# Performance work log

Measured on AMD Instinct MI355X. Metric: run time of the kernel, lower is better.

The kernel has to match this reference:

```python
import jax, jax.numpy as jnp
import numpy as np

B, T, D, H = 4, 4096, 2048, 128

def setup_inputs() -> dict:
    key = jax.random.key(0)
    k1, k2, k3, k4 = jax.random.split(key, 4)
    scale = 0.02
    return {
        "x": jax.random.normal(k1, (B, T, D), dtype=jnp.float32),
        "Wq": jax.random.normal(k2, (D, H), dtype=jnp.float32) * scale,
        "Wk": jax.random.normal(k3, (D, H), dtype=jnp.float32) * scale,
        "Wv": jax.random.normal(k4, (D, H), dtype=jnp.float32) * scale,
    }

def reference(x, Wq, Wk, Wv):
    # x: [B,T,D]; projections to [B,T,H]
    q = jnp.einsum('btd,dh->bth', x, Wq)
    k = jnp.einsum('btd,dh->bth', x, Wk)
    v = jnp.einsum('btd,dh->bth', x, Wv)
    scale = 1.0 / jnp.sqrt(jnp.asarray(q.shape[-1], q.dtype))
    scores = jnp.einsum('bth,bsh->bts', q, k) * scale  # [B,T,T]
    t = x.shape[1]
    causal = jnp.tril(jnp.ones((t, t), dtype=bool))
    scores = jnp.where(causal, scores, -jnp.inf)
    weights = jax.nn.softmax(scores, axis=-1)
    # dropout p=0.0 (eval) -> identity
    out = jnp.einsum('bts,bsh->bth', weights, v)
    return out
```

## Files before the change

kernel.cpp:

```cpp
#include <hip/hip_runtime.h>
#include <hip/hip_bf16.h>

#define Bq 4
#define Tq 4096
#define Dq 2048
#define Hq 128
#define Mq (Bq*Tq)
#define CHUNK 16

typedef __attribute__((ext_vector_type(8))) short bf16x8;
typedef __attribute__((ext_vector_type(4))) float f32x4;

static __device__ __forceinline__ short bfbits(float f) {
    union { __hip_bfloat16 h; short s; } u;
    u.h = __float2bfloat16(f);
    return u.s;
}
static __device__ __forceinline__ float bf2f(short s) {
    union { unsigned u; float f; } v;
    v.u = ((unsigned)(unsigned short)s) << 16;
    return v.f;
}
#define WAIT_LDS() __builtin_amdgcn_s_waitcnt(0xC07F)

__global__ __launch_bounds__(256, 1) void wt_kernel(
    const float* __restrict__ Wqp,
    const float* __restrict__ Wkp,
    const float* __restrict__ Wvp,
    short* __restrict__ wTg)
{
    __shared__ short trsp[128][136];
    const int kc = blockIdx.x;
    const int w  = blockIdx.y;
    const float* __restrict__ W = (w == 0) ? Wqp : (w == 1) ? Wkp : Wvp;
    const float scale = (w == 0) ? 0.08838834764831843f : 1.0f;
    const int t = threadIdx.x;

    #pragma unroll
    for (int i = 0; i < 16; i++) {
        int idx = t + i * 256;
        int r = idx >> 5, c4 = idx & 31;
        float4 f = *(const float4*)&W[(size_t)(kc * 128 + r) * Hq + c4 * 4];
        trsp[c4 * 4 + 0][r] = bfbits(f.x * scale);
        trsp[c4 * 4 + 1][r] = bfbits(f.y * scale);
        trsp[c4 * 4 + 2][r] = bfbits(f.z * scale);
        trsp[c4 * 4 + 3][r] = bfbits(f.w * scale);
    }
    __syncthreads();
    #pragma unroll
    for (int i = 0; i < 8; i++) {
        int idx = t + i * 256;
        int h = idx >> 4, c8 = idx & 15;
        *(bf16x8*)&wTg[((size_t)w * 128 + h) * Dq + kc * 128 + c8 * 8] =
            *(bf16x8*)&trsp[h][c8 * 8];
    }
}

__global__ __launch_bounds__(256, 2) void qkv_fused_kernel(
    const float* __restrict__ x,
    const short* __restrict__ wTg,
    short* __restrict__ qg,
    short* __restrict__ kg,
    short* __restrict__ vTt)
{
    __shared__ short smem[32 * 72 + 384 * 72];
    short (*xs)[72]  = (short(*)[72])smem;
    short (*wts)[72] = (short(*)[72])(smem + 32 * 72);

    const int m0 = blockIdx.x * 32;

    const int t    = threadIdx.x;
    const int lane = t & 63;
    const int qw   = t >> 6;
    const int l15  = lane & 15;
    const int quad = lane >> 4;

    f32x4 o[2][6];
    #pragma unroll
    for (int mf = 0; mf < 2; mf++)
        #pragma unroll
        for (int j = 0; j < 6; j++) o[mf][j] = (f32x4){0.f, 0.f, 0.f, 0.f};

    const int xr = t >> 3, xc = (t & 7) * 8;

    float4  xreg[2];
    bf16x8  wreg[12];

    {
        const float* src = x + (size_t)(m0 + xr) * Dq + xc;
        xreg[0] = *(const float4*)(src + 0);
        xreg[1] = *(const float4*)(src + 4);
        #pragma unroll
        for (int i = 0; i < 12; i++) {
            int idx = t + i * 256;
            wreg[i] = *(const bf16x8*)&wTg[(size_t)(idx >> 3) * Dq + (idx & 7) * 8];
        }
        bf16x8 v0;
        v0[0] = bfbits(xreg[0].x); v0[1] = bfbits(xreg[0].y);
        v0[2] = bfbits(xreg[0].z); v0[3] = bfbits(xreg[0].w);
        v0[4] = bfbits(xreg[1].x); v0[5] = bfbits(xreg[1].y);
        v0[6] = bfbits(xreg[1].z); v0[7] = bfbits(xreg[1].w);
        *(bf16x8*)&xs[xr][xc] = v0;
        #pragma unroll
        for (int i = 0; i < 12; i++) {
            int idx = t + i * 256;
            *(bf16x8*)&wts[idx >> 3][(idx & 7) * 8] = wreg[i];
        }
    }
    __syncthreads();

    for (int k0 = 0; k0 < Dq; k0 += 64) {
        if (k0 + 64 < Dq) {
            const float* src = x + (size_t)(m0 + xr) * Dq + k0 + 64 + xc;
            xreg[0] = *(const float4*)(src + 0);
            xreg[1] = *(const float4*)(src + 4);
            #pragma unroll
            for (int i = 0; i < 12; i++) {
                int idx = t + i * 256;
                wreg[i] = *(const bf16x8*)&wTg[(size_t)(idx >> 3) * Dq + k0 + 64 + (idx & 7) * 8];
            }
        }

        #pragma unroll
        for (int kk = 0; kk < 2; kk++) {
            bf16x8 a[2], b[6];
            #pragma unroll
            for (int mf = 0; mf < 2; mf++)
                a[mf] = *(bf16x8*)&xs[mf * 16 + l15][kk * 32 + quad * 8];
            #pragma unroll
            for (int j = 0; j < 6; j++)
                b[j] = *(bf16x8*)&wts[qw * 96 + j * 16 + l15][kk * 32 + quad * 8];
            #pragma unroll
            for (int mf = 0; mf < 2; mf++)
                #pragma unroll
                for (int j = 0; j < 6; j++)
                    o[mf][j] = __builtin_amdgcn_mfma_f32_16x16x32_bf16(
                        a[mf], b[j], o[mf][j], 0, 0, 0);
        }
        __syncthreads();
        if (k0 + 64 < Dq) {
            bf16x8 v0;
            v0[0] = bfbits(xreg[0].x); v0[1] = bfbits(xreg[0].y);
            v0[2] = bfbits(xreg[0].z); v0[3] = bfbits(xreg[0].w);
            v0[4] = bfbits(xreg[1].x); v0[5] = bfbits(xreg[1].y);
            v0[6] = bfbits(xreg[1].z); v0[7] = bfbits(xreg[1].w);
            *(bf16x8*)&xs[xr][xc] = v0;
            #pragma unroll
            for (int i = 0; i < 12; i++) {
                int idx = t + i * 256;
                *(bf16x8*)&wts[idx >> 3][(idx & 7) * 8] = wreg[i];
            }
            __syncthreads();
        }
    }

    {
        short (*e64)[264] = (short(*)[264])smem;
        #pragma unroll
        for (int mf = 0; mf < 2; mf++)
            #pragma unroll
            for (int j = 0; j < 6; j++) {
                int n0 = qw * 96 + j * 16;
                if (n0 < 256) {
                    #pragma unroll
                    for (int reg = 0; reg < 4; reg++)
                        e64[mf * 16 + quad * 4 + reg][n0 + l15] = bfbits(o[mf][j][reg]);
                }
            }
        __syncthreads();
        #pragma unroll
        for (int i = 0; i < 4; i++) {
            int idx = t + i * 256;
            int r = idx >> 5, u = idx & 31;
            int n = u * 8;
            bf16x8 val = *(bf16x8*)&e64[r][n];
            short* dst = (n < 128) ? &qg[(size_t)(m0 + r) * Hq + n]
                                   : &kg[(size_t)(m0 + r) * Hq + (n - 128)];
            *(bf16x8*)dst = val;
        }
    }
    __syncthreads();
    {
        short (*e128)[40] = (short(*)[40])smem;
        #pragma unroll
        for (int mf = 0; mf < 2; mf++)
            #pragma unroll
            for (int j = 0; j < 6; j++) {
                int n0 = qw * 96 + j * 16;
                if (n0 >= 256) {
                    short4 pk;
                    pk.x = bfbits(o[mf][j][0]); pk.y = bfbits(o[mf][j][1]);
                    pk.z = bfbits(o[mf][j][2]); pk.w = bfbits(o[mf][j][3]);
                    *(short4*)&e128[(n0 - 256) + l15][mf * 16 + quad * 4] = pk;
                }
            }
        __syncthreads();
        const int bb   = m0 / Tq;
        const int jt   = (m0 % Tq) >> 6;
        const int moff = m0 & 63;
        #pragma unroll
        for (int i = 0; i < 2; i++) {
            int idx = t + i * 256;
            int h = idx >> 2, u = idx & 3;
            *(bf16x8*)&vTt[(((size_t)bb * (Tq / 64) + jt) * 128 + h) * 64 + moff + u * 8] =
                *(bf16x8*)&e128[h][u * 8];
        }
    }
}

__global__ __launch_bounds__(256, 3) void attn_part_kernel(
    const short* __restrict__ qg, const short* __restrict__ kg,
    const short* __restrict__ vTt,
    short* __restrict__ Opart,
    float* __restrict__ lv)
{
    __shared__ short ks_s[64][136];
    __shared__ short vt_s[128][72];
    __shared__ short ps_s[64][72];

    const int qt = blockIdx.x;
    const int b  = blockIdx.y;
    const int c  = blockIdx.z;
    const int q0 = qt * 64;

    const int lo = c * CHUNK;
    const int hi = min(qt + 1, lo + CHUNK);
    if (lo >= hi) return;

    const int t    = threadIdx.x;
    const int lane = t & 63;
    const int qw   = t >> 6;
    const int l15  = lane & 15;
    const int quad = lane >> 4;

    bf16x8 qf[4];
    {
        const short* qsrc = qg + (size_t)(b * Tq + q0 + qw * 16 + l15) * Hq + quad * 8;
        #pragma unroll
        for (int kk = 0; kk < 4; kk++)
            qf[kk] = *(const bf16x8*)(qsrc + kk * 32);
    }

    float lsum[4] = {0.f, 0.f, 0.f, 0.f};
    f32x4 o[8];
    #pragma unroll
    for (int nf = 0; nf < 8; nf++) o[nf] = (f32x4){0.f, 0.f, 0.f, 0.f};

    bf16x8 kreg[4], vreg[4];
    {
        const size_t kbase = (size_t)(b * Tq + lo * 64) * Hq;
        const short* vsrc = vTt + (((size_t)b * (Tq / 64) + lo) * 128) * 64;
        #pragma unroll
        for (int i = 0; i < 4; i++) {
            int idx = t + i * 256;
            kreg[i] = *(const bf16x8*)&kg[kbase + (size_t)(idx >> 4) * Hq + (idx & 15) * 8];
            vreg[i] = *(const bf16x8*)&vsrc[idx * 8];
        }
        #pragma unroll
        for (int i = 0; i < 4; i++) {
            int idx = t + i * 256;
            *(bf16x8*)&ks_s[idx >> 4][(idx & 15) * 8] = kreg[i];
            *(bf16x8*)&vt_s[idx >> 3][(idx & 7) * 8]  = vreg[i];
        }
    }
    __syncthreads();

    for (int jt = lo; jt < hi; jt++) {
        if (jt + 1 < hi) {
            const size_t kbase = (size_t)(b * Tq + (jt + 1) * 64) * Hq;
            const short* vsrc = vTt + (((size_t)b * (Tq / 64) + jt + 1) * 128) * 64;
            #pragma unroll
            for (int i = 0; i < 4; i++) {
                int idx = t + i * 256;
                kreg[i] = *(const bf16x8*)&kg[kbase + (size_t)(idx >> 4) * Hq + (idx & 15) * 8];
                vreg[i] = *(const bf16x8*)&vsrc[idx * 8];
            }
        }

        f32x4 sacc[4];
        #pragma unroll
        for (int nf = 0; nf < 4; nf++) sacc[nf] = (f32x4){0.f, 0.f, 0.f, 0.f};
        #pragma unroll
        for (int kk = 0; kk < 4; kk++) {
            bf16x8 bk[4];
            #pragma unroll
            for (int nf = 0; nf < 4; nf++)
                bk[nf] = *(bf16x8*)&ks_s[nf * 16 + l15][kk * 32 + quad * 8];
            #pragma unroll
            for (int nf = 0; nf < 4; nf++)
                sacc[nf] = __builtin_amdgcn_mfma_f32_16x16x32_bf16(qf[kk], bk[nf], sacc[nf], 0, 0, 0);
        }

        const bool diag = (jt == qt);
        #pragma unroll
        for (int reg = 0; reg < 4; reg++) {
            const int rloc = qw * 16 + quad * 4 + reg;
            #pragma unroll
            for (int nf = 0; nf < 4; nf++) {
                float s = sacc[nf][reg];
                if (diag && (nf * 16 + l15 > rloc)) s = -1e30f;
                float p = __expf(s);
                lsum[reg] += p;
                ps_s[rloc][nf * 16 + l15] = bfbits(p);
            }
        }
        WAIT_LDS();

        #pragma unroll
        for (int ks2 = 0; ks2 < 2; ks2++) {
            bf16x8 ap = *(bf16x8*)&ps_s[qw * 16 + l15][ks2 * 32 + quad * 8];
            bf16x8 bv[8];
            #pragma unroll
            for (int nf = 0; nf < 8; nf++)
                bv[nf] = *(bf16x8*)&vt_s[nf * 16 + l15][ks2 * 32 + quad * 8];
            #pragma unroll
            for (int nf = 0; nf < 8; nf++)
                o[nf] = __builtin_amdgcn_mfma_f32_16x16x32_bf16(ap, bv[nf], o[nf], 0, 0, 0);
        }

        __syncthreads();
        if (jt + 1 < hi) {
            #pragma unroll
            for (int i = 0; i < 4; i++) {
                int idx = t + i * 256;
                *(bf16x8*)&ks_s[idx >> 4][(idx & 15) * 8] = kreg[i];
                *(bf16x8*)&vt_s[idx >> 3][(idx & 7) * 8]  = vreg[i];
            }
            __syncthreads();
        }
    }

    #pragma unroll
    for (int reg = 0; reg < 4; reg++) {
        #pragma unroll
        for (int mm = 8; mm >= 1; mm >>= 1)
            lsum[reg] += __shfl_xor(lsum[reg], mm, 16);
    }
    const size_t zoff = (size_t)c * Mq;
    if (l15 == 0) {
        #pragma unroll
        for (int reg = 0; reg < 4; reg++)
            lv[zoff + (size_t)b * Tq + q0 + qw * 16 + quad * 4 + reg] = lsum[reg];
    }

    __syncthreads();
    short (*epi)[136] = (short(*)[136])&ks_s[0][0];
    #pragma unroll
    for (int nf = 0; nf < 8; nf++)
        #pragma unroll
        for (int reg = 0; reg < 4; reg++)
            epi[qw * 16 + quad * 4 + reg][nf * 16 + l15] = bfbits(o[nf][reg]);
    __syncthreads();
    #pragma unroll
    for (int i = 0; i < 4; i++) {
        int idx = t + i * 256;
        int r = idx >> 4, cc = idx & 15;
        *(bf16x8*)&Opart[(zoff + (size_t)b * Tq + q0 + r) * Hq + cc * 8] =
            *(bf16x8*)&epi[r][cc * 8];
    }
}

__global__ __launch_bounds__(256, 4) void merge_kernel(
    const short* __restrict__ Opart, const float* __restrict__ lv,
    float* __restrict__ outg)
{
    const int t   = threadIdx.x;
    const int row = blockIdx.x * 16 + (t >> 4);
    const int cu  = t & 15;

    const int rl  = row & (Tq - 1);
    const int nch = (rl >> 10) + 1;

    float lsum = 0.f;
    float acc[8] = {};
    for (int cc = 0; cc < nch; cc++) {
        lsum += lv[(size_t)cc * Mq + row];
        bf16x8 oc = *(const bf16x8*)&Opart[((size_t)cc * Mq + row) * Hq + cu * 8];
        #pragma unroll
        for (int j = 0; j < 8; j++) acc[j] += bf2f(oc[j]);
    }
    float inv = 1.0f / lsum;

    float4 r0, r1;
    r0.x = acc[0] * inv; r0.y = acc[1] * inv; r0.z = acc[2] * inv; r0.w = acc[3] * inv;
    r1.x = acc[4] * inv; r1.y = acc[5] * inv; r1.z = acc[6] * inv; r1.w = acc[7] * inv;
    float* dst = &outg[(size_t)row * Hq + cu * 8];
    *(float4*)dst       = r0;
    *(float4*)(dst + 4) = r1;
}

extern "C" void kernel_launch(void* const* d_in, const int* in_sizes, int n_in,
                              void* d_out, int out_size, void* d_ws, size_t ws_size,
                              hipStream_t stream) {
    const float* x   = (const float*)d_in[0];
    const float* Wqp = (const float*)d_in[1];
    const float* Wkp = (const float*)d_in[2];
    const float* Wvp = (const float*)d_in[3];
    float* out = (float*)d_out;

    short* qg    = (short*)d_ws;
    short* kg    = qg  + (size_t)Mq * Hq;
    short* vTt   = kg  + (size_t)Mq * Hq;
    short* Opart = vTt + (size_t)Mq * Hq;
    short* wTg   = Opart;
    float* lv    = (float*)(Opart + (size_t)4 * Mq * Hq);

    wt_kernel<<<dim3(16, 3), dim3(256), 0, stream>>>(Wqp, Wkp, Wvp, wTg);
    qkv_fused_kernel<<<dim3(Mq / 32), dim3(256), 0, stream>>>(x, wTg, qg, kg, vTt);
    attn_part_kernel<<<dim3(Tq / 64, Bq, 4), dim3(256), 0, stream>>>(qg, kg, vTt, Opart, lv);
    merge_kernel<<<dim3(Mq / 16), dim3(256), 0, stream>>>(Opart, lv, out);
}
```

Baseline: 278.6 us.

## Rework QKV projection to async global-to-LDS double buffering with 64-row tiles

The QKV projection kernel now uses 512 threads over 64-row tiles. Tiles of x (fp32) and weights are loaded straight into swizzled, double-buffered LDS with global_load_lds, and the loop waits on vmcnt, replacing the register staging path. Conversion of x to bf16 moves from the store side to the LDS read before the MFMA, and each weight tile is reused across twice as many rows. This aims to overlap memory traffic with MFMA work and halve weight reloads. In exchange it uses 128KB of LDS, which limits occupancy, and x data in LDS takes twice the space as fp32.

```diff
diff --git a/kernel.cpp b/kernel.cpp
--- a/kernel.cpp
+++ b/kernel.cpp
@@ -22,6 +22,12 @@
     return v.f;
 }
 #define WAIT_LDS() __builtin_amdgcn_s_waitcnt(0xC07F)
+
+static __device__ __forceinline__ void gload16(const void* g, void* l) {
+    __builtin_amdgcn_global_load_lds(
+        (const __attribute__((address_space(1))) unsigned int*)g,
+        (__attribute__((address_space(3))) unsigned int*)l, 16, 0, 0);
+}
 
 __global__ __launch_bounds__(256, 1) void wt_kernel(
     const float* __restrict__ Wqp,
@@ -56,24 +62,23 @@
     }
 }
 
-__global__ __launch_bounds__(256, 2) void qkv_fused_kernel(
+__global__ __launch_bounds__(512, 2) void qkv_fused_kernel(
     const float* __restrict__ x,
     const short* __restrict__ wTg,
     short* __restrict__ qg,
     short* __restrict__ kg,
     short* __restrict__ vTt)
 {
-    __shared__ short smem[32 * 72 + 384 * 72];
-    short (*xs)[72]  = (short(*)[72])smem;
-    short (*wts)[72] = (short(*)[72])(smem + 32 * 72);
-
-    const int m0 = blockIdx.x * 32;
-
+    __shared__ __attribute__((aligned(128))) char smem[131072];
+
+    const int m0   = blockIdx.x * 64;
     const int t    = threadIdx.x;
-    const int lane = t & 63;
-    const int qw   = t >> 6;
-    const int l15  = lane & 15;
-    const int quad = lane >> 4;
+    const int l    = t & 63;
+    const int w    = t >> 6;
+    const int l15  = l & 15;
+    const int quad = l >> 4;
+    const int wm   = (w >> 2) * 32;
+    const int wn   = (w & 3) * 96;
 
     f32x4 o[2][6];
     #pragma unroll
@@ -81,78 +86,77 @@
         #pragma unroll
         for (int j = 0; j < 6; j++) o[mf][j] = (f32x4){0.f, 0.f, 0.f, 0.f};
 
-    const int xr = t >> 3, xc = (t & 7) * 8;
-
-    float4  xreg[2];
-    bf16x8  wreg[12];
-
-    {
-        const float* src = x + (size_t)(m0 + xr) * Dq + xc;
-        xreg[0] = *(const float4*)(src + 0);
-        xreg[1] = *(const float4*)(src + 4);
-        #pragma unroll
-        for (int i = 0; i < 12; i++) {
-            int idx = t + i * 256;
-            wreg[i] = *(const bf16x8*)&wTg[(size_t)(idx >> 3) * Dq + (idx & 7) * 8];
-        }
-        bf16x8 v0;
-        v0[0] = bfbits(xreg[0].x); v0[1] = bfbits(xreg[0].y);
-        v0[2] = bfbits(xreg[0].z); v0[3] = bfbits(xreg[0].w);
-        v0[4] = bfbits(xreg[1].x); v0[5] = bfbits(xreg[1].y);
-        v0[6] = bfbits(xreg[1].z); v0[7] = bfbits(xreg[1].w);
-        *(bf16x8*)&xs[xr][xc] = v0;
-        #pragma unroll
-        for (int i = 0; i < 12; i++) {
-            int idx = t + i * 256;
-            *(bf16x8*)&wts[idx >> 3][(idx & 7) * 8] = wreg[i];
-        }
-    }
-    __syncthreads();
-
-    for (int k0 = 0; k0 < Dq; k0 += 64) {
-        if (k0 + 64 < Dq) {
-            const float* src = x + (size_t)(m0 + xr) * Dq + k0 + 64 + xc;
-            xreg[0] = *(const float4*)(src + 0);
-            xreg[1] = *(const float4*)(src + 4);
-            #pragma unroll
-            for (int i = 0; i < 12; i++) {
-                int idx = t + i * 256;
-                wreg[i] = *(const bf16x8*)&wTg[(size_t)(idx >> 3) * Dq + k0 + 64 + (idx & 7) * 8];
-            }
-        }
-
+    const short* wsrcb = wTg + (size_t)(w * 48 + (l >> 3)) * Dq
+                             + (((l & 7) ^ ((l >> 3) & 7)) << 3);
+    const int xr0 = w * 8 + (l >> 4);
+
+    #define QKV_STAGE(it2, buf)                                                  \
+        do {                                                                     \
+            const int k0_ = (it2) * 64;                                          \
+            char* xb_ = smem + (buf) * 65536;                                    \
+            char* wb_ = xb_ + 16384;                                             \
+            _Pragma("unroll")                                                    \
+            for (int j2 = 0; j2 < 2; j2++) {                                     \
+                int r_ = xr0 + j2 * 4;                                           \
+                int kbs_ = ((l & 15) ^ (r_ & 15)) << 4;                          \
+                gload16((const char*)(x + (size_t)(m0 + r_) * Dq + k0_) + kbs_,  \
+                        xb_ + (w * 2 + j2) * 1024);                              \
+            }                                                                    \
+            _Pragma("unroll")                                                    \
+            for (int j = 0; j < 6; j++)                                          \
+                gload16(wsrcb + (size_t)j * 8 * Dq + k0_,                        \
+                        wb_ + (w * 6 + j) * 1024);                               \
+        } while (0)
+
+    QKV_STAGE(0, 0);
+    QKV_STAGE(1, 1);
+
+    #pragma unroll 2
+    for (int it = 0; it < 32; ++it) {
+        if (it < 31) asm volatile("s_waitcnt vmcnt(8)" ::: "memory");
+        else         asm volatile("s_waitcnt vmcnt(0)" ::: "memory");
+        __builtin_amdgcn_s_barrier();
+        __builtin_amdgcn_sched_barrier(0);
+
+        const char* xb = smem + (it & 1) * 65536;
+        const char* wb = xb + 16384;
         #pragma unroll
         for (int kk = 0; kk < 2; kk++) {
-            bf16x8 a[2], b[6];
-            #pragma unroll
-            for (int mf = 0; mf < 2; mf++)
-                a[mf] = *(bf16x8*)&xs[mf * 16 + l15][kk * 32 + quad * 8];
-            #pragma unroll
-            for (int j = 0; j < 6; j++)
-                b[j] = *(bf16x8*)&wts[qw * 96 + j * 16 + l15][kk * 32 + quad * 8];
+            bf16x8 a[2];
+            #pragma unroll
+            for (int mf = 0; mf < 2; mf++) {
+                int rm = wm + mf * 16 + l15;
+                int sh = (rm & 15) << 4;
+                int kb = kk * 128 + quad * 32;
+                f32x4 f0 = *(const f32x4*)(xb + rm * 256 + ((kb     ) ^ sh));
+                f32x4 f1 = *(const f32x4*)(xb + rm * 256 + ((kb + 16) ^ sh));
+                bf16x8 af;
+                af[0] = bfbits(f0[0]); af[1] = bfbits(f0[1]);
+                af[2] = bfbits(f0[2]); af[3] = bfbits(f0[3]);
+                af[4] = bfbits(f1[0]); af[5] = bfbits(f1[1]);
+                af[6] = bfbits(f1[2]); af[7] = bfbits(f1[3]);
+                a[mf] = af;
+            }
+            bf16x8 bw[6];
+            #pragma unroll
+            for (int j = 0; j < 6; j++) {
+                int n = wn + j * 16 + l15;
+                bw[j] = *(const bf16x8*)(wb + n * 128 +
+                        ((kk * 64 + quad * 16) ^ ((n & 7) << 4)));
+            }
             #pragma unroll
             for (int mf = 0; mf < 2; mf++)
                 #pragma unroll
                 for (int j = 0; j < 6; j++)
                     o[mf][j] = __builtin_amdgcn_mfma_f32_16x16x32_bf16(
-                        a[mf], b[j], o[mf][j], 0, 0, 0);
-        }
-        __syncthreads();
-        if (k0 + 64 < Dq) {
-            bf16x8 v0;
-            v0[0] = bfbits(xreg[0].x); v0[1] = bfbits(xreg[0].y);
-            v0[2] = bfbits(xreg[0].z); v0[3] = bfbits(xreg[0].w);
-            v0[4] = bfbits(xreg[1].x); v0[5] = bfbits(xreg[1].y);
-            v0[6] = bfbits(xreg[1].z); v0[7] = bfbits(xreg[1].w);
-            *(bf16x8*)&xs[xr][xc] = v0;
-            #pragma unroll
-            for (int i = 0; i < 12; i++) {
-                int idx = t + i * 256;
-                *(bf16x8*)&wts[idx >> 3][(idx & 7) * 8] = wreg[i];
-            }
-            __syncthreads();
-        }
-    }
+                        a[mf], bw[j], o[mf][j], 0, 0, 0);
+        }
+
+        __builtin_amdgcn_s_barrier();
+        __builtin_amdgcn_sched_barrier(0);
+        if (it < 30) QKV_STAGE(it + 2, it & 1);
+    }
+    #undef QKV_STAGE
 
     {
         short (*e64)[264] = (short(*)[264])smem;
@@ -160,17 +164,17 @@
         for (int mf = 0; mf < 2; mf++)
             #pragma unroll
             for (int j = 0; j < 6; j++) {
-                int n0 = qw * 96 + j * 16;
+                int n0 = wn + j * 16;
                 if (n0 < 256) {
                     #pragma unroll
                     for (int reg = 0; reg < 4; reg++)
-                        e64[mf * 16 + quad * 4 + reg][n0 + l15] = bfbits(o[mf][j][reg]);
+                        e64[wm + mf * 16 + quad * 4 + reg][n0 + l15] = bfbits(o[mf][j][reg]);
                 }
             }
         __syncthreads();
         #pragma unroll
         for (int i = 0; i < 4; i++) {
-            int idx = t + i * 256;
+            int idx = t + i * 512;
             int r = idx >> 5, u = idx & 31;
             int n = u * 8;
             bf16x8 val = *(bf16x8*)&e64[r][n];
@@ -181,28 +185,27 @@
     }
     __syncthreads();
     {
-        short (*e128)[40] = (short(*)[40])smem;
+        short (*e128)[72] = (short(*)[72])smem;
         #pragma unroll
         for (int mf = 0; mf < 2; mf++)
             #pragma unroll
             for (int j = 0; j < 6; j++) {
-                int n0 = qw * 96 + j * 16;
+                int n0 = wn + j * 16;
                 if (n0 >= 256) {
                     short4 pk;
                     pk.x = bfbits(o[mf][j][0]); pk.y = bfbits(o[mf][j][1]);
                     pk.z = bfbits(o[mf][j][2]); pk.w = bfbits(o[mf][j][3]);
-                    *(short4*)&e128[(n0 - 256) + l15][mf * 16 + quad * 4] = pk;
+                    *(short4*)&e128[(n0 - 256) + l15][wm + mf * 16 + quad * 4] = pk;
                 }
             }
         __syncthreads();
-        const int bb   = m0 / Tq;
-        const int jt   = (m0 % Tq) >> 6;
-        const int moff = m0 & 63;
+        const int bb = m0 / Tq;
+        const int jt = (m0 % Tq) >> 6;
         #pragma unroll
         for (int i = 0; i < 2; i++) {
-            int idx = t + i * 256;
-            int h = idx >> 2, u = idx & 3;
-            *(bf16x8*)&vTt[(((size_t)bb * (Tq / 64) + jt) * 128 + h) * 64 + moff + u * 8] =
+            int idx = t + i * 512;
+            int h = idx >> 3, u = idx & 7;
+            *(bf16x8*)&vTt[(((size_t)bb * (Tq / 64) + jt) * 128 + h) * 64 + u * 8] =
                 *(bf16x8*)&e128[h][u * 8];
         }
     }
@@ -406,7 +409,7 @@
     float* lv    = (float*)(Opart + (size_t)4 * Mq * Hq);
 
     wt_kernel<<<dim3(16, 3), dim3(256), 0, stream>>>(Wqp, Wkp, Wvp, wTg);
-    qkv_fused_kernel<<<dim3(Mq / 32), dim3(256), 0, stream>>>(x, wTg, qg, kg, vTt);
+    qkv_fused_kernel<<<dim3(Mq / 64), dim3(512), 0, stream>>>(x, wTg, qg, kg, vTt);
     attn_part_kernel<<<dim3(Tq / 64, Bq, 4), dim3(256), 0, stream>>>(qg, kg, vTt, Opart, lv);
     merge_kernel<<<dim3(Mq / 16), dim3(256), 0, stream>>>(Opart, lv, out);
 }
```

Result: faster. 265.4 us (-4.8%).
